# Kernel tuning notes

Hardware: AMD Instinct MI355X
Metric: run time of the kernel (lower is better)

Reference implementation:

```python
import jax, jax.numpy as jnp
import numpy as np
from jax import lax

N = 20000        # nodes
E = 320000       # directed edges (avg degree 16)
F_IN = 512       # input feature dim
HID = 64         # hidden_layer
K_NEI = 8        # sampled neighbors per node
L = K_NEI + 1    # local subgraph size (self + neighbors)
N_TPL = 10       # N_templates
NT = 8           # N_templates_nodes
N_CLS = 6
ALPHA = 0.5      # FGW trade-off
EPS = 0.1        # entropic regularization
N_OUTER = 3      # outer CG iterations
N_SINK = 5       # sinkhorn iterations per outer step


def setup_inputs() -> dict:
    rng = np.random.default_rng(0)
    src = rng.integers(0, N, E).astype(np.int64)
    dst = rng.integers(0, N, E).astype(np.int64)
    edge_index = np.stack([src, dst])

    # fixed-size neighbor table (pad with self, mask)
    nbr = np.full((N, K_NEI), -1, np.int64)
    cnt = np.zeros(N, np.int64)
    for s, d in zip(src, dst):
        c = cnt[s]
        if c < K_NEI:
            nbr[s, c] = d
            cnt[s] = c + 1
    pad = nbr < 0
    self_col = np.arange(N, dtype=np.int64)
    nbr = np.where(pad, self_col[:, None], nbr)
    nbr_mask = np.concatenate([np.ones((N, 1)), (~pad).astype(np.float64)], 1).astype(np.float32)

    # local adjacency among {self, neighbors}: [N, L, L]
    idx_full = np.concatenate([self_col[:, None], nbr], 1)  # [N, L]
    edge_keys = np.unique(src * N + dst)
    keys = idx_full[:, :, None] * N + idx_full[:, None, :]
    C_local = np.isin(keys, edge_keys).astype(np.float32)

    ks = jax.random.split(jax.random.key(0), 10)
    x = jax.random.normal(ks[0], (N, F_IN), jnp.float32)
    W1 = jax.random.normal(ks[1], (F_IN, HID), jnp.float32) / np.float32(np.sqrt(F_IN))
    b1 = jnp.zeros((HID,), jnp.float32)
    W2 = jax.random.normal(ks[2], (HID, HID), jnp.float32) / np.float32(np.sqrt(HID))
    b2 = jnp.zeros((HID,), jnp.float32)
    t = jax.random.uniform(ks[3], (N_TPL, NT, NT), jnp.float32)
    templates = 0.5 * (t + jnp.swapaxes(t, 1, 2))  # symmetric template adjacency
    templates_features = jax.random.normal(ks[4], (N_TPL, NT, HID), jnp.float32)
    Wlin = jax.random.normal(ks[5], (HID + N_TPL, N_CLS), jnp.float32) / np.float32(np.sqrt(HID + N_TPL))
    blin = jnp.zeros((N_CLS,), jnp.float32)
    return {"x": x, "edge_index": jnp.asarray(edge_index), "nbr_idx": jnp.asarray(nbr),
            "nbr_mask": jnp.asarray(nbr_mask), "C_local": jnp.asarray(C_local),
            "W1": W1, "b1": b1, "W2": W2, "b2": b2,
            "templates": templates, "templates_features": templates_features,
            "Wlin": Wlin, "blin": blin}


def gcn(x, W, b, src, dst, n):
    xw = x @ W
    sl = jnp.arange(n)
    s = jnp.concatenate([src, sl])
    d = jnp.concatenate([dst, sl])
    deg = jax.ops.segment_sum(jnp.ones_like(s, jnp.float32), d, num_segments=n)
    dinv = lax.rsqrt(deg)
    coef = dinv[s] * dinv[d]
    return jax.ops.segment_sum(xw[s] * coef[:, None], d, num_segments=n) + b


def fgw_dist(M, C1, h1, C2, h2):
    # entropic fused GW (square loss) with fixed iterations; padded rows have h1 = 0
    f1 = C1 * C1
    f2 = C2 * C2
    constC = (f1 @ h1)[:, None] + (f2 @ h2)[None, :]
    T0 = h1[:, None] * h2[None, :]

    def outer(T, _):
        tens = constC - 2.0 * (C1 @ T @ C2)
        G = (1.0 - ALPHA) * M + ALPHA * tens
        Kmat = jnp.exp(-G / EPS)

        def sink(carry, _):
            u, v = carry
            u = h1 / (Kmat @ v + 1e-16)
            v = h2 / (Kmat.T @ u + 1e-16)
            return (u, v), None

        (u, v), _ = lax.scan(sink, (jnp.ones_like(h1), jnp.ones_like(h2)), None, length=N_SINK)
        return u[:, None] * Kmat * v[None, :], None

    T, _ = lax.scan(outer, T0, None, length=N_OUTER)
    tens = constC - 2.0 * (C1 @ T @ C2)
    return jnp.sum(T * ((1.0 - ALPHA) * M + ALPHA * tens))


def distance_to_template(x, nbr_idx, nbr_mask, C_local, templates_features, templates):
    n = x.shape[0]
    idx_full = jnp.concatenate([jnp.arange(n)[:, None], nbr_idx], axis=1)  # [N, L]
    xl = x[idx_full]  # [N, L, HID]
    # squared euclidean cost to each template: [N, T, L, NT]
    inner = jnp.einsum('nld,tmd->ntlm', xl, templates_features)
    M = (jnp.sum(xl * xl, -1)[:, None, :, None]
         + jnp.sum(templates_features * templates_features, -1)[None, :, None, :]
         - 2.0 * inner)
    h1 = nbr_mask / jnp.sum(nbr_mask, -1, keepdims=True)  # [N, L]
    h2 = jnp.full((NT,), 1.0 / NT, jnp.float32)

    per_tpl = jax.vmap(fgw_dist, in_axes=(0, None, None, 0, None))
    per_node = jax.vmap(per_tpl, in_axes=(0, 0, 0, None, None))
    return per_node(M, C_local, h1, templates, h2)  # [N, N_TPL]


def reference(x, edge_index, nbr_idx, nbr_mask, C_local, W1, b1, W2, b2,
              templates, templates_features, Wlin, blin):
    src, dst = edge_index[0], edge_index[1]
    n = x.shape[0]
    h = jax.nn.relu(gcn(x, W1, b1, src, dst, n))
    h = gcn(h, W2, b2, src, dst, n)
    y = distance_to_template(h, nbr_idx, nbr_mask, C_local, templates_features, templates)
    out = jnp.concatenate([h, y], axis=1) @ Wlin + blin
    return jax.nn.relu(out)
```

## Files before the change

### kernel.cpp

```cpp
#include <hip/hip_runtime.h>


#define NN   20000
#define EE   320000
#define FIN  512
#define HID  64
#define KNEI 8
#define LSZ  9
#define NTPL 10
#define NTN  8
#define NCLS 6
#define CAP  48

typedef unsigned short bf16_t;
typedef unsigned short us8 __attribute__((ext_vector_type(8)));
typedef __bf16 bf16x8 __attribute__((ext_vector_type(8)));
typedef float f32x4 __attribute__((ext_vector_type(4)));

__device__ __forceinline__ float b2f(bf16_t u) {
  union { unsigned int i; float f; } v; v.i = ((unsigned int)u) << 16; return v.f;
}
__device__ __forceinline__ bf16_t f2b(float f) {
  union { float f; unsigned int i; } v; v.f = f;
  unsigned int x = v.i;
  return (bf16_t)((x + 0x7fffu + ((x >> 16) & 1u)) >> 16);
}
__device__ __forceinline__ float ldf(const void* p, long i, int fp32) {
  return fp32 ? ((const float*)p)[i] : b2f(((const bf16_t*)p)[i]);
}
__device__ __forceinline__ int ldi(const void* p, long i, int i64) {
  return i64 ? (int)((const long long*)p)[i] : ((const int*)p)[i];
}
__device__ __forceinline__ float frcp(float x) { return __builtin_amdgcn_rcpf(x); }

__global__ __launch_bounds__(128) void probe_kernel(const void* __restrict__ x,
                                                    const void* __restrict__ ei,
                                                    const void* __restrict__ tfeat,
                                                    int* __restrict__ flags,
                                                    float* __restrict__ tn2min) {
  __shared__ int sfl[2];
  __shared__ float tn2s[80];
  int tid = threadIdx.x;
  if (tid == 0) {
    int sane = 0;
    for (int k = 0; k < 64; k += 2) {
      bf16_t u = ((const bf16_t*)x)[k];
      int e = (u >> 7) & 0xff;
      if (e >= 112 && e <= 142) sane++;
    }
    int f0 = (sane < 24) ? 1 : 0;
    int zc = 0;
    for (int k = 1; k < 64; k += 2)
      if (((const int*)ei)[k] == 0) zc++;
    int f1 = (zc >= 16) ? 1 : 0;
    flags[0] = f0; flags[1] = f1;
    sfl[0] = f0; sfl[1] = f1;
  }
  __syncthreads();
  if (tid < 80) {
    int fF = sfl[0];
    float s = 0.f;
    for (int k = 0; k < HID; ++k) {
      float v = ldf(tfeat, (long)tid * HID + k, fF);
      s += v * v;
    }
    tn2s[tid] = s;
  }
  __syncthreads();
  if (tid == 0) {
    float gmin = 1e30f;
    for (int t = 0; t < NTPL; ++t) {
      float m = tn2s[t * 8];
      for (int r = 1; r < 8; ++r) m = fminf(m, tn2s[t * 8 + r]);
      tn2min[t] = m;
      gmin = fminf(gmin, m);
    }
    tn2min[NTPL] = gmin;
  }
}

__global__ __launch_bounds__(256) void scatter_kernel(const void* __restrict__ ei,
                                                      int* __restrict__ pos,
                                                      int* __restrict__ slot,
                                                      const int* __restrict__ flags) {
  int i = blockIdx.x * 256 + threadIdx.x;
  if (i >= EE) return;
  int i64 = flags[1];
  int s = ldi(ei, i, i64);
  int d = ldi(ei, (long)EE + i, i64);
  int p = atomicAdd(&pos[d], 1);
  if (p < CAP) slot[d * CAP + p] = s;
}

__global__ __launch_bounds__(512) void gemm1_kernel(const void* __restrict__ x,
                                                    const void* __restrict__ W1,
                                                    float* __restrict__ xw1,
                                                    const int* __restrict__ flags) {
  const int tid = threadIdx.x;
  const int wid = tid >> 6;
  const int lane = tid & 63;
  const int fF = flags[0];

  if (!fF) {
    __shared__ bf16_t wtS[HID * FIN];
    for (int i = tid; i < (FIN * HID) / 8; i += 512) {
      us8 v = ((const us8*)W1)[i];
      int k = i >> 3;
      int c0 = (i & 7) * 8;
#pragma unroll
      for (int q = 0; q < 8; ++q)
        wtS[(c0 + q) * FIN + (k ^ (q << 3))] = v[q];
    }
    __syncthreads();

    const int ct = wid & 3;
    const int ws = blockIdx.x * 2 + (wid >> 2);
    const int lr = lane & 15;
    const int lg = lane >> 4;

    bf16x8 af[16];
#pragma unroll
    for (int s = 0; s < 16; ++s) {
      int idx8 = (ct * 16 + lr) * (FIN / 8) + ((4 * s + lg) ^ (lane & 7));
      union { us8 u; bf16x8 b; } t;
      t.u = *(const us8*)&wtS[idx8 * 8];
      af[s] = t.b;
    }

    for (int rb = ws; rb < NN / 16; rb += 512) {
      const int row = rb * 16 + lr;
      const bf16x8* xp = (const bf16x8*)x + (long)row * (FIN / 8) + lg;
      f32x4 acc0 = {0.f, 0.f, 0.f, 0.f};
      f32x4 acc1 = {0.f, 0.f, 0.f, 0.f};
#pragma unroll
      for (int s = 0; s < 16; s += 2) {
        bf16x8 b0 = xp[4 * s];
        bf16x8 b1 = xp[4 * s + 4];
        acc0 = __builtin_amdgcn_mfma_f32_16x16x32_bf16(af[s], b0, acc0, 0, 0, 0);
        acc1 = __builtin_amdgcn_mfma_f32_16x16x32_bf16(af[s + 1], b1, acc1, 0, 0, 0);
      }
      f32x4 r = acc0 + acc1;
      *(f32x4*)&xw1[(long)row * HID + ct * 16 + lg * 4] = r;
    }
  } else {
    for (int row0 = (blockIdx.x * 8 + wid) * 4; row0 < NN; row0 += 2048 * 4) {
      float a0 = 0.f, a1 = 0.f, a2 = 0.f, a3 = 0.f;
      const float* x0 = (const float*)x + (long)row0 * FIN;
      const float* wp = (const float*)W1;
#pragma unroll 8
      for (int k = 0; k < FIN; ++k) {
        float w = wp[k * HID + lane];
        a0 += x0[k] * w;
        a1 += x0[FIN + k] * w;
        a2 += x0[2 * FIN + k] * w;
        a3 += x0[3 * FIN + k] * w;
      }
      xw1[(long)(row0 + 0) * HID + lane] = a0;
      xw1[(long)(row0 + 1) * HID + lane] = a1;
      xw1[(long)(row0 + 2) * HID + lane] = a2;
      xw1[(long)(row0 + 3) * HID + lane] = a3;
    }
  }
}

__global__ __launch_bounds__(256) void gatherA_kernel(const float* __restrict__ xw,
                                                      const int* __restrict__ cnt,
                                                      const int* __restrict__ slot,
                                                      float* __restrict__ xw2,
                                                      const void* __restrict__ b1v,
                                                      const void* __restrict__ W2,
                                                      const int* __restrict__ flags) {
  int n = blockIdx.x * 4 + (threadIdx.x >> 6);
  if (n >= NN) return;
  int fF = flags[0];
  int c = threadIdx.x & 63;
  float dn = rsqrtf((float)cnt[n] + 1.0f);
  float acc = xw[(long)n * HID + c] * dn;
  int m = cnt[n]; if (m > CAP) m = CAP;
  const int* sl = slot + (long)n * CAP;
  float accB = 0.f;
  for (int e0 = 0; e0 < m; e0 += 8) {
    int4 sa = *(const int4*)(sl + e0);
    int4 sb = *(const int4*)(sl + e0 + 4);
    if (e0 + 0 < m) acc  += xw[(long)sa.x * HID + c] * rsqrtf((float)cnt[sa.x] + 1.0f);
    if (e0 + 1 < m) accB += xw[(long)sa.y * HID + c] * rsqrtf((float)cnt[sa.y] + 1.0f);
    if (e0 + 2 < m) acc  += xw[(long)sa.z * HID + c] * rsqrtf((float)cnt[sa.z] + 1.0f);
    if (e0 + 3 < m) accB += xw[(long)sa.w * HID + c] * rsqrtf((float)cnt[sa.w] + 1.0f);
    if (e0 + 4 < m) acc  += xw[(long)sb.x * HID + c] * rsqrtf((float)cnt[sb.x] + 1.0f);
    if (e0 + 5 < m) accB += xw[(long)sb.y * HID + c] * rsqrtf((float)cnt[sb.y] + 1.0f);
    if (e0 + 6 < m) acc  += xw[(long)sb.z * HID + c] * rsqrtf((float)cnt[sb.z] + 1.0f);
    if (e0 + 7 < m) accB += xw[(long)sb.w * HID + c] * rsqrtf((float)cnt[sb.w] + 1.0f);
  }
  float h1 = (acc + accB) * dn + ldf(b1v, c, fF);
  h1 = h1 > 0.f ? h1 : 0.f;

  float o = 0.f;
#pragma unroll 8
  for (int k = 0; k < HID; ++k)
    o += __shfl(h1, k) * ldf(W2, k * HID + c, fF);
  xw2[(long)n * HID + c] = o;
}

__global__ __launch_bounds__(256) void gatherB_kernel(const float* __restrict__ xw,
                                                      const int* __restrict__ cnt,
                                                      const int* __restrict__ slot,
                                                      float* __restrict__ h,
                                                      float* __restrict__ n2,
                                                      const void* __restrict__ b2v,
                                                      const int* __restrict__ flags) {
  int n = blockIdx.x * 4 + (threadIdx.x >> 6);
  if (n >= NN) return;
  int c = threadIdx.x & 63;
  float dn = rsqrtf((float)cnt[n] + 1.0f);
  float acc = xw[(long)n * HID + c] * dn;
  int m = cnt[n]; if (m > CAP) m = CAP;
  const int* sl = slot + (long)n * CAP;
  float accB = 0.f;
  for (int e0 = 0; e0 < m; e0 += 8) {
    int4 sa = *(const int4*)(sl + e0);
    int4 sb = *(const int4*)(sl + e0 + 4);
    if (e0 + 0 < m) acc  += xw[(long)sa.x * HID + c] * rsqrtf((float)cnt[sa.x] + 1.0f);
    if (e0 + 1 < m) accB += xw[(long)sa.y * HID + c] * rsqrtf((float)cnt[sa.y] + 1.0f);
    if (e0 + 2 < m) acc  += xw[(long)sa.z * HID + c] * rsqrtf((float)cnt[sa.z] + 1.0f);
    if (e0 + 3 < m) accB += xw[(long)sa.w * HID + c] * rsqrtf((float)cnt[sa.w] + 1.0f);
    if (e0 + 4 < m) acc  += xw[(long)sb.x * HID + c] * rsqrtf((float)cnt[sb.x] + 1.0f);
    if (e0 + 5 < m) accB += xw[(long)sb.y * HID + c] * rsqrtf((float)cnt[sb.y] + 1.0f);
    if (e0 + 6 < m) acc  += xw[(long)sb.z * HID + c] * rsqrtf((float)cnt[sb.z] + 1.0f);
    if (e0 + 7 < m) accB += xw[(long)sb.w * HID + c] * rsqrtf((float)cnt[sb.w] + 1.0f);
  }
  acc = (acc + accB) * dn;
  h[(long)n * HID + c] = acc;
  float v = acc + ldf(b2v, c, flags[0]);
  float s = v * v;
  s += __shfl_xor(s, 1); s += __shfl_xor(s, 2); s += __shfl_xor(s, 4);
  s += __shfl_xor(s, 8); s += __shfl_xor(s, 16); s += __shfl_xor(s, 32);
  if (c == 0) n2[n] = s;
}

#define NODES_PB 4
#define TPN 80
#define XLP 65

__global__ __launch_bounds__(320, 2) void fgw_kernel(
    const float* __restrict__ h2,
    const void* __restrict__ b2v,
    const void* __restrict__ nbr_idx,
    const void* __restrict__ nbr_mask,
    const void* __restrict__ C_local,
    const void* __restrict__ tmpl,
    const void* __restrict__ tfeat,
    const void* __restrict__ Wlin,
    const void* __restrict__ blin,
    void* __restrict__ out,
    const int* __restrict__ flags,
    const float* __restrict__ tn2min,
    const float* __restrict__ n2)
{
  const int tid = threadIdx.x;
  const int fF = flags[0];
  const int fI = flags[1];
  const int nb = tid / TPN;
  const int local = tid - nb * TPN;
  const int t = local >> 3;
  const int j = local & 7;
  const int n = blockIdx.x * NODES_PB + nb;
  const int lane = tid & 63;
  const int ob = lane & 56;

  __shared__ float xlS[NODES_PB][LSZ][XLP];
  __shared__ float C1S[NODES_PB][81];
  __shared__ float hwS[NODES_PB][LSZ];
  __shared__ float f1S[NODES_PB][LSZ];
  __shared__ float xnS[NODES_PB][LSZ];
  __shared__ float distS[NODES_PB][NTPL];
  __shared__ float xmaxS[NODES_PB];
  __shared__ int   needS[NODES_PB];
  __shared__ int   sidxS[NODES_PB][LSZ];
  __shared__ float WlinS[(HID + NTPL) * NCLS + NCLS];

  for (int i = tid; i < (HID + NTPL) * NCLS; i += 320)
    WlinS[i] = ldf(Wlin, i, fF);
  if (tid < NCLS) WlinS[(HID + NTPL) * NCLS + tid] = ldf(blin, tid, fF);

  if (local < LSZ) {
    int idx = (local == 0) ? n : ldi(nbr_idx, (long)n * KNEI + local - 1, fI);
    sidxS[nb][local] = idx;
    xnS[nb][local] = n2[idx];
  }
  if (local < HID)
    xlS[nb][0][local] = h2[(long)n * HID + local] + ldf(b2v, local, fF);
  __syncthreads();

  if (local == 0) {
    float xm = xnS[nb][0];
#pragma unroll
    for (int l = 1; l < LSZ; ++l) xm = fmaxf(xm, xnS[nb][l]);
    xmaxS[nb] = xm;
    needS[nb] = ((sqrtf(tn2min[NTPL]) - sqrtf(xm)) >= 5.0990195f) ? 0 : 1;
  }
  __syncthreads();

  const int need = needS[nb];
  if (need) {
    for (int i = local; i < 8 * HID; i += TPN) {
      int l = 1 + (i >> 6), k = i & 63;
      xlS[nb][l][k] = h2[(long)sidxS[nb][l] * HID + k] + ldf(b2v, k, fF);
    }
    for (int i = local; i < 81; i += TPN)
      C1S[nb][i] = ldf(C_local, (long)n * 81 + i, fF);
  }
  __syncthreads();

  if (need && local < LSZ) {
    int l = local;
    float msum = 0.f, f1 = 0.f;
#pragma unroll
    for (int jj = 0; jj < LSZ; ++jj) {
      float mj = ldf(nbr_mask, (long)n * LSZ + jj, fF);
      msum += mj;
      float c = C1S[nb][l * LSZ + jj];
      f1 += c * c * mj;
    }
    float inv = frcp(msum);
    hwS[nb][l] = ldf(nbr_mask, (long)n * LSZ + l, fF) * inv;
    f1S[nb][l] = f1 * inv;
  }
  __syncthreads();

  bool slow = need && ((sqrtf(tn2min[t]) - sqrtf(xmaxS[nb])) < 5.0990195f);
  if (slow) {
    float C2c[NTN];
    float f2h2;
    {
      float s = 0.f;
#pragma unroll
      for (int m = 0; m < NTN; ++m) {
        C2c[m] = ldf(tmpl, t * 64 + m * 8 + j, fF);
        float r = ldf(tmpl, t * 64 + j * 8 + m, fF);
        s += r * r;
      }
      f2h2 = s * 0.125f;
    }
    float hwr[LSZ], f1r[LSZ];
#pragma unroll
    for (int l = 0; l < LSZ; ++l) { hwr[l] = hwS[nb][l]; f1r[l] = f1S[nb][l]; }

    float Mc[LSZ];
    {
      float accI[LSZ];
#pragma unroll
      for (int l = 0; l < LSZ; ++l) accI[l] = 0.f;
      float tn2 = 0.f;
      const long tb = (long)local * HID;
      for (int kb = 0; kb < 8; ++kb) {
        float r[8];
#pragma unroll
        for (int q = 0; q < 8; ++q) r[q] = ldf(tfeat, tb + kb * 8 + q, fF);
#pragma unroll
        for (int q = 0; q < 8; ++q) tn2 += r[q] * r[q];
#pragma unroll
        for (int l = 0; l < LSZ; ++l) {
          float s = 0.f;
#pragma unroll
          for (int q = 0; q < 8; ++q) s += xlS[nb][l][kb * 8 + q] * r[q];
          accI[l] += s;
        }
      }
#pragma unroll
      for (int l = 0; l < LSZ; ++l)
        Mc[l] = xnS[nb][l] + tn2 - 2.f * accI[l];
    }

    float Tc[LSZ], Kc[LSZ], u[LSZ];
#pragma unroll
    for (int l = 0; l < LSZ; ++l) Tc[l] = hwr[l] * 0.125f;

    float v = 1.0f;
    for (int outer = 0; outer < 3; ++outer) {
      float Ac[LSZ];
#pragma unroll
      for (int l = 0; l < LSZ; ++l) {
        float s = 0.f;
#pragma unroll
        for (int l2 = 0; l2 < LSZ; ++l2) s += C1S[nb][l * LSZ + l2] * Tc[l2];
        Ac[l] = s;
      }
#pragma unroll
      for (int l = 0; l < LSZ; ++l) {
        float s = 0.f;
#pragma unroll
        for (int m = 0; m < NTN; ++m) s += __shfl(Ac[l], ob + m) * C2c[m];
        float tens = f1r[l] + f2h2 - 2.f * s;
        Kc[l] = __expf(-5.0f * (Mc[l] + tens));
      }
      v = 1.0f;
      for (int it = 0; it < 5; ++it) {
#pragma unroll
        for (int l = 0; l < LSZ; ++l) {
          float p = Kc[l] * v;
          p += __shfl_xor(p, 1); p += __shfl_xor(p, 2); p += __shfl_xor(p, 4);
          u[l] = hwr[l] * frcp(p + 1e-16f);
        }
        float s = 0.f;
#pragma unroll
        for (int l = 0; l < LSZ; ++l) s += Kc[l] * u[l];
        v = 0.125f * frcp(s + 1e-16f);
      }
#pragma unroll
      for (int l = 0; l < LSZ; ++l) Tc[l] = u[l] * Kc[l] * v;
    }
    {
      float Ac[LSZ];
#pragma unroll
      for (int l = 0; l < LSZ; ++l) {
        float s = 0.f;
#pragma unroll
        for (int l2 = 0; l2 < LSZ; ++l2) s += C1S[nb][l * LSZ + l2] * Tc[l2];
        Ac[l] = s;
      }
      float cl = 0.f;
#pragma unroll
      for (int l = 0; l < LSZ; ++l) {
        float s = 0.f;
#pragma unroll
        for (int m = 0; m < NTN; ++m) s += __shfl(Ac[l], ob + m) * C2c[m];
        float tens = f1r[l] + f2h2 - 2.f * s;
        cl += Tc[l] * 0.5f * (Mc[l] + tens);
      }
      cl += __shfl_xor(cl, 1); cl += __shfl_xor(cl, 2); cl += __shfl_xor(cl, 4);
      if (j == 0) distS[nb][t] = cl;
    }
  } else if (j == 0) {
    distS[nb][t] = 0.f;
  }
  __syncthreads();

  if (local < NCLS) {
    int c = local;
    float acc = WlinS[(HID + NTPL) * NCLS + c];
#pragma unroll
    for (int k = 0; k < HID; ++k)
      acc += xlS[nb][0][k] * WlinS[k * NCLS + c];
#pragma unroll
    for (int tt = 0; tt < NTPL; ++tt)
      acc += distS[nb][tt] * WlinS[(HID + tt) * NCLS + c];
    float r = acc > 0.f ? acc : 0.f;
    if (fF) ((float*)out)[(long)n * NCLS + c] = r;
    else    ((bf16_t*)out)[(long)n * NCLS + c] = f2b(r);
  }
}

extern "C" void kernel_launch(void* const* d_in, const int* in_sizes, int n_in,
                              void* d_out, int out_size, void* d_ws, size_t ws_size,
                              hipStream_t stream) {
  (void)in_sizes; (void)n_in; (void)out_size; (void)ws_size;
  const void* x     = d_in[0];
  const void* ei    = d_in[1];
  const void* nbr   = d_in[2];
  const void* nmask = d_in[3];
  const void* Cl    = d_in[4];
  const void* W1    = d_in[5];
  const void* b1    = d_in[6];
  const void* W2    = d_in[7];
  const void* b2    = d_in[8];
  const void* tmpl  = d_in[9];
  const void* tfeat = d_in[10];
  const void* Wlin  = d_in[11];
  const void* blin  = d_in[12];

  int*   flags  = (int*)d_ws;
  float* tn2min = (float*)d_ws + 4;
  float* n2     = (float*)d_ws + 16;
  int*   pos    = (int*)(n2 + NN);
  int*   slot   = pos + NN;
  float* bufA   = (float*)(slot + (long)CAP * NN);
  float* bufB   = bufA + (long)NN * HID;

  probe_kernel<<<1, 128, 0, stream>>>(x, ei, tfeat, flags, tn2min);

  hipMemsetAsync(pos, 0, NN * sizeof(int), stream);
  scatter_kernel<<<(EE + 255) / 256, 256, 0, stream>>>(ei, pos, slot, flags);

  gemm1_kernel<<<256, 512, 0, stream>>>(x, W1, bufA, flags);
  gatherA_kernel<<<NN / 4, 256, 0, stream>>>(bufA, pos, slot, bufB, b1, W2, flags);
  gatherB_kernel<<<NN / 4, 256, 0, stream>>>(bufB, pos, slot, bufA, n2, b2, flags);

  fgw_kernel<<<NN / NODES_PB, 320, 0, stream>>>(bufA, b2, nbr, nmask, Cl, tmpl,
                                                tfeat, Wlin, blin, d_out, flags,
                                                tn2min, n2);
}
```

Before: 335.1 us.

## Pre-transpose W1 in a separate kernel and launch one gemm1 block per row tile

Adds a small wt_kernel that writes a transposed bf16 copy of W1 to workspace once. gemm1 then has each block handle one 16-row tile, with each of its four waves loading its W1 fragments straight from global or L2 instead of every block building a 64KB transposed LDS copy. The old kernel used a persistent grid of 256 blocks with large LDS use. The new grid has 1250 small blocks with no LDS, which removes the per-block staging cost and raises occupancy. In exchange, A fragments are re-read from cache per tile, and there is one extra kernel launch.

```diff
diff --git a/kernel.cpp b/kernel.cpp
--- a/kernel.cpp
+++ b/kernel.cpp
@@ -92,74 +92,77 @@
   if (p < CAP) slot[d * CAP + p] = s;
 }
 
-__global__ __launch_bounds__(512) void gemm1_kernel(const void* __restrict__ x,
-                                                    const void* __restrict__ W1,
-                                                    float* __restrict__ xw1,
-                                                    const int* __restrict__ flags) {
+__global__ __launch_bounds__(256) void wt_kernel(const void* __restrict__ W1,
+                                                 bf16_t* __restrict__ w1t,
+                                                 const int* __restrict__ flags) {
+  if (flags[0]) return;
+  __shared__ bf16_t tile[HID][HID + 2];
+  const int b = blockIdx.x;
+  const int tid = threadIdx.x;
+  const bf16_t* w = (const bf16_t*)W1;
+  for (int i = tid; i < 512; i += 256) {
+    int kk = i >> 3, c8 = i & 7;
+    us8 v = *(const us8*)&w[(long)(64 * b + kk) * HID + c8 * 8];
+#pragma unroll
+    for (int q = 0; q < 8; ++q) tile[c8 * 8 + q][kk] = v[q];
+  }
+  __syncthreads();
+  for (int i = tid; i < 512; i += 256) {
+    int c = i >> 3, j = i & 7;
+    us8 v;
+#pragma unroll
+    for (int q = 0; q < 8; ++q) v[q] = tile[c][j * 8 + q];
+    *(us8*)&w1t[(long)c * FIN + 64 * b + j * 8] = v;
+  }
+}
+
+__global__ __launch_bounds__(256, 2) void gemm1_kernel(const void* __restrict__ x,
+                                                       const bf16_t* __restrict__ w1t,
+                                                       const void* __restrict__ W1,
+                                                       float* __restrict__ xw1,
+                                                       const int* __restrict__ flags) {
   const int tid = threadIdx.x;
   const int wid = tid >> 6;
   const int lane = tid & 63;
-  const int fF = flags[0];
-
-  if (!fF) {
-    __shared__ bf16_t wtS[HID * FIN];
-    for (int i = tid; i < (FIN * HID) / 8; i += 512) {
-      us8 v = ((const us8*)W1)[i];
-      int k = i >> 3;
-      int c0 = (i & 7) * 8;
-#pragma unroll
-      for (int q = 0; q < 8; ++q)
-        wtS[(c0 + q) * FIN + (k ^ (q << 3))] = v[q];
-    }
-    __syncthreads();
-
-    const int ct = wid & 3;
-    const int ws = blockIdx.x * 2 + (wid >> 2);
+
+  if (!flags[0]) {
+    const int ct = wid;
     const int lr = lane & 15;
     const int lg = lane >> 4;
-
-    bf16x8 af[16];
-#pragma unroll
-    for (int s = 0; s < 16; ++s) {
-      int idx8 = (ct * 16 + lr) * (FIN / 8) + ((4 * s + lg) ^ (lane & 7));
-      union { us8 u; bf16x8 b; } t;
-      t.u = *(const us8*)&wtS[idx8 * 8];
-      af[s] = t.b;
-    }
-
-    for (int rb = ws; rb < NN / 16; rb += 512) {
-      const int row = rb * 16 + lr;
-      const bf16x8* xp = (const bf16x8*)x + (long)row * (FIN / 8) + lg;
-      f32x4 acc0 = {0.f, 0.f, 0.f, 0.f};
-      f32x4 acc1 = {0.f, 0.f, 0.f, 0.f};
-#pragma unroll
-      for (int s = 0; s < 16; s += 2) {
-        bf16x8 b0 = xp[4 * s];
-        bf16x8 b1 = xp[4 * s + 4];
-        acc0 = __builtin_amdgcn_mfma_f32_16x16x32_bf16(af[s], b0, acc0, 0, 0, 0);
-        acc1 = __builtin_amdgcn_mfma_f32_16x16x32_bf16(af[s + 1], b1, acc1, 0, 0, 0);
-      }
-      f32x4 r = acc0 + acc1;
-      *(f32x4*)&xw1[(long)row * HID + ct * 16 + lg * 4] = r;
-    }
+    const int row = blockIdx.x * 16 + lr;
+    const bf16x8* xp = (const bf16x8*)x + (long)row * (FIN / 8) + lg;
+    const bf16x8* ap = (const bf16x8*)w1t + (long)(ct * 16 + lr) * (FIN / 8) + lg;
+    f32x4 acc0 = {0.f, 0.f, 0.f, 0.f};
+    f32x4 acc1 = {0.f, 0.f, 0.f, 0.f};
+#pragma unroll
+    for (int s = 0; s < 16; s += 2) {
+      bf16x8 a0 = ap[4 * s];
+      bf16x8 b0 = xp[4 * s];
+      bf16x8 a1 = ap[4 * s + 4];
+      bf16x8 b1 = xp[4 * s + 4];
+      acc0 = __builtin_amdgcn_mfma_f32_16x16x32_bf16(a0, b0, acc0, 0, 0, 0);
+      acc1 = __builtin_amdgcn_mfma_f32_16x16x32_bf16(a1, b1, acc1, 0, 0, 0);
+    }
+    f32x4 r = acc0 + acc1;
+    *(f32x4*)&xw1[(long)row * HID + ct * 16 + lg * 4] = r;
   } else {
-    for (int row0 = (blockIdx.x * 8 + wid) * 4; row0 < NN; row0 += 2048 * 4) {
-      float a0 = 0.f, a1 = 0.f, a2 = 0.f, a3 = 0.f;
-      const float* x0 = (const float*)x + (long)row0 * FIN;
-      const float* wp = (const float*)W1;
+    int row0 = (blockIdx.x * 4 + wid) * 4;
+    if (row0 >= NN) return;
+    float a0 = 0.f, a1 = 0.f, a2 = 0.f, a3 = 0.f;
+    const float* x0 = (const float*)x + (long)row0 * FIN;
+    const float* wp = (const float*)W1;
 #pragma unroll 8
-      for (int k = 0; k < FIN; ++k) {
-        float w = wp[k * HID + lane];
-        a0 += x0[k] * w;
-        a1 += x0[FIN + k] * w;
-        a2 += x0[2 * FIN + k] * w;
-        a3 += x0[3 * FIN + k] * w;
-      }
-      xw1[(long)(row0 + 0) * HID + lane] = a0;
-      xw1[(long)(row0 + 1) * HID + lane] = a1;
-      xw1[(long)(row0 + 2) * HID + lane] = a2;
-      xw1[(long)(row0 + 3) * HID + lane] = a3;
-    }
+    for (int k = 0; k < FIN; ++k) {
+      float w = wp[k * HID + lane];
+      a0 += x0[k] * w;
+      a1 += x0[FIN + k] * w;
+      a2 += x0[2 * FIN + k] * w;
+      a3 += x0[3 * FIN + k] * w;
+    }
+    xw1[(long)(row0 + 0) * HID + lane] = a0;
+    xw1[(long)(row0 + 1) * HID + lane] = a1;
+    xw1[(long)(row0 + 2) * HID + lane] = a2;
+    xw1[(long)(row0 + 3) * HID + lane] = a3;
   }
 }
 
@@ -468,20 +471,22 @@
   const void* Wlin  = d_in[11];
   const void* blin  = d_in[12];
 
-  int*   flags  = (int*)d_ws;
-  float* tn2min = (float*)d_ws + 4;
-  float* n2     = (float*)d_ws + 16;
-  int*   pos    = (int*)(n2 + NN);
-  int*   slot   = pos + NN;
-  float* bufA   = (float*)(slot + (long)CAP * NN);
-  float* bufB   = bufA + (long)NN * HID;
+  int*    flags  = (int*)d_ws;
+  float*  tn2min = (float*)d_ws + 4;
+  float*  n2     = (float*)d_ws + 16;
+  int*    pos    = (int*)(n2 + NN);
+  int*    slot   = pos + NN;
+  float*  bufA   = (float*)(slot + (long)CAP * NN);
+  float*  bufB   = bufA + (long)NN * HID;
+  bf16_t* w1t    = (bf16_t*)(bufB + (long)NN * HID);
 
   probe_kernel<<<1, 128, 0, stream>>>(x, ei, tfeat, flags, tn2min);
 
   hipMemsetAsync(pos, 0, NN * sizeof(int), stream);
+  wt_kernel<<<8, 256, 0, stream>>>(W1, w1t, flags);
   scatter_kernel<<<(EE + 255) / 256, 256, 0, stream>>>(ei, pos, slot, flags);
 
-  gemm1_kernel<<<256, 512, 0, stream>>>(x, W1, bufA, flags);
+  gemm1_kernel<<<NN / 16, 256, 0, stream>>>(x, w1t, W1, bufA, flags);
   gatherA_kernel<<<NN / 4, 256, 0, stream>>>(bufA, pos, slot, bufB, b1, W2, flags);
   gatherB_kernel<<<NN / 4, 256, 0, stream>>>(bufB, pos, slot, bufA, n2, b2, flags);
 
```

Result: faster. 315.8 us (-5.8%).
